# Kernel optimization log

Hardware: AMD Instinct MI355X
Metric: run time of the kernel (lower is better)

Reference implementation:

```python
import jax, jax.numpy as jnp
import numpy as np

B, K, N, D, H, NNEG, NTOP = 8, 8, 128, 256, 128, 64, 64
UNARY_SCALES = (1.0, 1.0, 1.0)  # one scale per tree level, tree_height = log2(K) = 3


def setup_inputs():
    key = jax.random.key(0)
    ks = jax.random.split(key, 8)
    s = 0.05
    return {
        'pos_fea': jax.random.normal(ks[0], (B, K, N, D), jnp.float32),
        'neg_fea': jax.random.normal(ks[1], (B * K, NNEG, D), jnp.float32),
        'pos_classes': jax.random.randint(ks[2], (B, K, N), 0, 20),
        'target_class': jax.random.randint(ks[3], (B,), 0, 20),
        'Wp1': jax.random.normal(ks[4], (2 * D, H), jnp.float32) * s,
        'bp1': jnp.zeros((H,), jnp.float32),
        'Wp2': jax.random.normal(ks[5], (H, 1), jnp.float32) * s,
        'bp2': jnp.zeros((1,), jnp.float32),
        'Wu1': jax.random.normal(ks[6], (2 * D, H), jnp.float32) * s,
        'bu1': jnp.zeros((H,), jnp.float32),
        'Wu2': jax.random.normal(ks[7], (H, 1), jnp.float32) * s,
        'bu2': jnp.zeros((1,), jnp.float32),
    }


def _relation(f0, f1, W1, b1, W2, b2):
    # RelationModule: Dense(H, relu) -> Dense(1) applied to concat([f0_m, f1_n])
    # for every cross pair; concat-Dense is split into two GEMMs. -> [Bn, M0, M1]
    d = f0.shape[-1]
    h0 = jnp.einsum('bmd,dh->bmh', f0, W1[:d])
    h1 = jnp.einsum('bnd,dh->bnh', f1, W1[d:])
    h = jax.nn.relu(h0[:, :, None, :] + h1[:, None, :, :] + b1)
    return jnp.einsum('bmnh,h->bmn', h, W2[:, 0]) + b2[0]


def _bg(t, idx):
    # batched_gather along axis 1: t [Bn, P, ...], idx [Bn, T]
    ie = idx.reshape(idx.shape + (1,) * (t.ndim - 2))
    ie = jnp.broadcast_to(ie, idx.shape + t.shape[2:])
    return jnp.take_along_axis(t, ie, axis=1)


def _rep(fea, sub):
    # subproblem representative feature: fea [Bn,S,N,D], sub [Bn,M,S] -> [Bn,M,D]
    idx = jnp.swapaxes(sub, 1, 2)[..., None]              # [Bn,S,M,1]
    idx = jnp.broadcast_to(idx, idx.shape[:-1] + (fea.shape[-1],))
    return jnp.take_along_axis(fea, idx, axis=2).mean(axis=1)


def _tree(pos_fea, neg_fea, Wp1, bp1, Wp2, bp2, Wu1, bu1, Wu2, bu2):
    pos_flat = pos_fea.reshape(B * K, N, D)
    # UnaryModule: mean relation score of each positive proposal vs the negative bag
    ue = _relation(pos_flat, neg_fea, Wu1, bu1, Wu2, bu2).mean(-1)   # [B*K, N]
    sub = jnp.broadcast_to(jnp.arange(N, dtype=jnp.int32)[None, :, None], (B * K, N, 1))
    pe = jnp.zeros_like(ue)
    tree_height = int(np.log2(K))
    best = None
    for i in range(tree_height):
        S = 2 ** i                      # subproblem size per branch at this level
        Bn = sub.shape[0] // 2
        M = sub.shape[1]
        sub2 = sub.reshape(Bn, 2, M, S)  # [::2] / [1::2] split of adjacent rows
        sub0, sub1 = sub2[:, 0], sub2[:, 1]
        pe2 = pe.reshape(Bn, 2, M)
        ue2 = ue.reshape(Bn, 2, M)
        fea = pos_flat.reshape(Bn, 2, S, N, D)
        rep0 = _rep(fea[:, 0], sub0)
        rep1 = _rep(fea[:, 1], sub1)
        # PairwiseCrossSimilarity: scores for all cross pairs of candidates
        scores = _relation(rep0, rep1, Wp1, bp1, Wp2, bp2).reshape(Bn, M * M)
        p0 = jnp.repeat(jnp.arange(M), M)
        p1 = jnp.tile(jnp.arange(M), M)
        pe = pe2[:, 0][:, p0] + pe2[:, 1][:, p1] - scores
        ue = ue2[:, 0][:, p0] + ue2[:, 1][:, p1]
        total = pe + UNARY_SCALES[i] * ue
        sub = jnp.concatenate([sub0[:, p0], sub1[:, p1]], axis=-1)  # [Bn, M*M, 2S]
        topk = 1 if i == tree_height - 1 else min(M * M, NTOP)
        _, inds = jax.lax.top_k(-total, topk)
        sub = _bg(sub, inds)
        ue = jnp.take_along_axis(ue, inds, axis=1)
        pe = jnp.take_along_axis(pe, inds, axis=1)
        best = jnp.take_along_axis(total, inds, axis=1)
    return sub, best


def reference(pos_fea, neg_fea, pos_classes, target_class,
              Wp1, bp1, Wp2, bp2, Wu1, bu1, Wu2, bu2):
    sub, _ = _tree(pos_fea, neg_fea, Wp1, bp1, Wp2, bp2, Wu1, bu1, Wu2, bu2)
    is_target = (pos_classes == target_class[:, None, None]).astype(jnp.float32)
    return sub[:, 0], is_target  # selected proposal per image [B,K], [B,K,N]
```

## Files before the change

kernel.cpp:

```cpp
#include <hip/hip_runtime.h>
#include <stdint.h>

#define B_ 8
#define K_ 8
#define N_ 128
#define D_ 256
#define H_ 128
#define NNEG_ 64

typedef unsigned long long u64;

__device__ __forceinline__ u64 shfl_xor_u64(u64 v, int m) {
    int lo = __shfl_xor((int)(unsigned)v, m, 64);
    int hi = __shfl_xor((int)(unsigned)(v >> 32), m, 64);
    return ((u64)(unsigned)hi << 32) | (unsigned)lo;
}
__device__ __forceinline__ u64 bitonic_merge64(u64 m, int lane) {
#pragma unroll
    for (int j = 32; j > 0; j >>= 1) {
        u64 o = shfl_xor_u64(m, j);
        bool keepMin = ((lane & j) == 0);
        bool lt = m < o;
        m = (keepMin == lt) ? m : o;
    }
    return m;
}
__device__ __forceinline__ unsigned sortable(float f) {
    unsigned u = __float_as_uint(f);
    return (u & 0x80000000u) ? ~u : (u | 0x80000000u);
}
__device__ __forceinline__ float unsortable(unsigned u) {
    return __uint_as_float((u & 0x80000000u) ? (u & 0x7FFFFFFFu) : ~u);
}
__device__ __forceinline__ void sort128_wave0(u64* cand, int cc, int lane) {
    u64 v0 = (lane < cc) ? cand[lane] : ~0ull;
    u64 v1 = (64 + lane < cc) ? cand[64 + lane] : ~0ull;
#pragma unroll
    for (int k = 2; k <= 64; k <<= 1) {
        bool d0 = ((lane & k) == 0);
        bool d1 = (k == 64) ? false : d0;
#pragma unroll
        for (int j = k >> 1; j > 0; j >>= 1) {
            u64 o0 = shfl_xor_u64(v0, j);
            bool km0 = (((lane & j) == 0) == d0);
            v0 = (km0 == (v0 < o0)) ? v0 : o0;
            u64 o1 = shfl_xor_u64(v1, j);
            bool km1 = (((lane & j) == 0) == d1);
            v1 = (km1 == (v1 < o1)) ? v1 : o1;
        }
    }
    if (v0 > v1) { u64 tmp = v0; v0 = v1; v1 = tmp; }
#pragma unroll
    for (int j = 32; j > 0; j >>= 1) {
        bool km = ((lane & j) == 0);
        u64 o0 = shfl_xor_u64(v0, j);
        v0 = (km == (v0 < o0)) ? v0 : o0;
        u64 o1 = shfl_xor_u64(v1, j);
        v1 = (km == (v1 < o1)) ? v1 : o1;
    }
    cand[lane] = v0; cand[64 + lane] = v1;
}

__global__ __launch_bounds__(256) void g1_gemm(
    const float* __restrict__ pos, const float* __restrict__ neg,
    const float* __restrict__ Wu1, const float* __restrict__ Wp1,
    const int* __restrict__ pos_classes, const int* __restrict__ target_class,
    float* __restrict__ HU0, float* __restrict__ HU1n,
    float* __restrict__ HP0, float* __restrict__ HP1,
    float* __restrict__ outp) {
    int bid = blockIdx.x;
    int t = threadIdx.x;
    if (bid >= 448) {
        int base = (bid - 448) * 2048 + t * 8;
#pragma unroll
        for (int q = 0; q < 8; ++q) {
            int idx = base + q;
            outp[64 + idx] = (pos_classes[idx] == target_class[idx >> 10]) ? 1.0f : 0.0f;
        }
        return;
    }
    const float* A; const float* W; float* OUT; int rb;
    if (bid < 128)      { A = pos; W = Wu1;           OUT = HU0;  rb = bid * 64; }
    else if (bid < 192) { A = neg; W = Wu1 + D_ * H_; OUT = HU1n; rb = (bid - 128) * 64; }
    else if (bid < 320) { A = pos; W = Wp1;           OUT = HP0;  rb = (bid - 192) * 64; }
    else                { A = pos; W = Wp1 + D_ * H_; OUT = HP1;  rb = (bid - 320) * 64; }

    __shared__ float As[64][17];
    __shared__ float Bs[16][128];
    int tx = t & 15, ty = t >> 4;
    float acc[4][8];
#pragma unroll
    for (int i = 0; i < 4; ++i)
#pragma unroll
        for (int j = 0; j < 8; ++j) acc[i][j] = 0.f;

    for (int k0 = 0; k0 < D_; k0 += 16) {
        {
            int row = t >> 2, kq = (t & 3) * 4;
            const float4 av = *(const float4*)&A[(size_t)(rb + row) * D_ + k0 + kq];
            As[row][kq + 0] = av.x; As[row][kq + 1] = av.y;
            As[row][kq + 2] = av.z; As[row][kq + 3] = av.w;
        }
        {
            int flat = t * 8;
            int kr = flat >> 7, hc = flat & 127;
            float4 b0 = *(const float4*)&W[(size_t)(k0 + kr) * H_ + hc];
            float4 b1 = *(const float4*)&W[(size_t)(k0 + kr) * H_ + hc + 4];
            *(float4*)&Bs[kr][hc] = b0;
            *(float4*)&Bs[kr][hc + 4] = b1;
        }
        __syncthreads();
#pragma unroll
        for (int kk = 0; kk < 16; ++kk) {
            float a0 = As[ty * 4 + 0][kk], a1 = As[ty * 4 + 1][kk];
            float a2 = As[ty * 4 + 2][kk], a3 = As[ty * 4 + 3][kk];
            float bv[8];
            *(float4*)&bv[0] = *(const float4*)&Bs[kk][tx * 8];
            *(float4*)&bv[4] = *(const float4*)&Bs[kk][tx * 8 + 4];
#pragma unroll
            for (int j = 0; j < 8; ++j) {
                acc[0][j] += a0 * bv[j];
                acc[1][j] += a1 * bv[j];
                acc[2][j] += a2 * bv[j];
                acc[3][j] += a3 * bv[j];
            }
        }
        __syncthreads();
    }
#pragma unroll
    for (int i = 0; i < 4; ++i) {
        float4 o0 = {acc[i][0], acc[i][1], acc[i][2], acc[i][3]};
        float4 o1 = {acc[i][4], acc[i][5], acc[i][6], acc[i][7]};
        *(float4*)&OUT[(size_t)(rb + ty * 4 + i) * H_ + tx * 8] = o0;
        *(float4*)&OUT[(size_t)(rb + ty * 4 + i) * H_ + tx * 8 + 4] = o1;
    }
}

__global__ __launch_bounds__(256) void g2_ue_sc0(
    const float* __restrict__ HU0, const float* __restrict__ HU1n,
    const float* __restrict__ bu1, const float* __restrict__ Wu2,
    const float* __restrict__ bu2v,
    const float* __restrict__ HP0, const float* __restrict__ HP1,
    const float* __restrict__ bp1, const float* __restrict__ Wp2,
    const float* __restrict__ bp2,
    float* __restrict__ t0, float* __restrict__ sc0) {
    __shared__ float smem[13568];
    float (*Ls)[129] = (float(*)[129])smem;
    float (*Rs)[129] = (float(*)[129])(smem + 4128);
    float* wsv = smem + 4128 + 8256;
    float (*red)[33] = (float(*)[33])(smem + 4128 + 8256 + 128);

    int bid = blockIdx.x;
    int t = threadIdx.x;
    bool is_ue = bid < 256;

    if (is_ue) {
        int bk = bid >> 2, mt = bid & 3;
        for (int i = t; i < 64 * 128; i += 256) {
            int n = i >> 7, h = i & 127;
            Rs[n][h] = HU1n[(size_t)(bk * NNEG_ + n) * H_ + h];
        }
        for (int i = t; i < 32 * 128; i += 256) {
            int m = i >> 7, h = i & 127;
            Ls[m][h] = HU0[(size_t)(bk * N_ + mt * 32 + m) * H_ + h] + bu1[h];
        }
        if (t < 128) wsv[t] = Wu2[t];
    } else {
        int bid2 = bid - 256;
        int b = bid2 >> 3, m0t = (bid2 >> 1) & 3, m1t = bid2 & 1;
        const float* Lg = HP0 + (size_t)b * 2 * N_ * H_ + m0t * 32 * H_;
        const float* Rg = HP1 + (size_t)b * 2 * N_ * H_ + N_ * H_ + m1t * 64 * H_;
        for (int i = t; i < 64 * 128; i += 256) {
            int n = i >> 7, h = i & 127;
            Rs[n][h] = Rg[(size_t)n * H_ + h];
        }
        for (int i = t; i < 32 * 128; i += 256) {
            int m = i >> 7, h = i & 127;
            Ls[m][h] = Lg[(size_t)m * H_ + h] + bp1[h];
        }
        if (t < 128) wsv[t] = Wp2[t];
    }
    __syncthreads();

    int tm = t & 7, tn = t >> 3;
    const float* l0 = &Ls[tm * 4 + 0][0];
    const float* l1 = &Ls[tm * 4 + 1][0];
    const float* l2 = &Ls[tm * 4 + 2][0];
    const float* l3 = &Ls[tm * 4 + 3][0];
    const float* r0 = &Rs[tn * 2 + 0][0];
    const float* r1 = &Rs[tn * 2 + 1][0];
    float a00 = 0.f, a01 = 0.f, a10 = 0.f, a11 = 0.f;
    float a20 = 0.f, a21 = 0.f, a30 = 0.f, a31 = 0.f;
#pragma unroll 4
    for (int h = 0; h < 128; ++h) {
        float w = wsv[h];
        float b0 = r0[h], b1 = r1[h];
        float a0 = l0[h], a1 = l1[h], a2 = l2[h], a3 = l3[h];
        float v;
        v = a0 + b0; v = v > 0.f ? v : 0.f; a00 += v * w;
        v = a0 + b1; v = v > 0.f ? v : 0.f; a01 += v * w;
        v = a1 + b0; v = v > 0.f ? v : 0.f; a10 += v * w;
        v = a1 + b1; v = v > 0.f ? v : 0.f; a11 += v * w;
        v = a2 + b0; v = v > 0.f ? v : 0.f; a20 += v * w;
        v = a2 + b1; v = v > 0.f ? v : 0.f; a21 += v * w;
        v = a3 + b0; v = v > 0.f ? v : 0.f; a30 += v * w;
        v = a3 + b1; v = v > 0.f ? v : 0.f; a31 += v * w;
    }

    if (is_ue) {
        int bk = bid >> 2, mt = bid & 3;
        red[tm * 4 + 0][tn] = a00 + a01;
        red[tm * 4 + 1][tn] = a10 + a11;
        red[tm * 4 + 2][tn] = a20 + a21;
        red[tm * 4 + 3][tn] = a30 + a31;
        __syncthreads();
        if (t < 32) {
            float s = 0.f;
            for (int q = 0; q < 32; ++q) s += red[t][q];
            t0[bk * N_ + mt * 32 + t] = s * (1.0f / NNEG_) + bu2v[0];
        }
    } else {
        int bid2 = bid - 256;
        int b = bid2 >> 3, m0t = (bid2 >> 1) & 3, m1t = bid2 & 1;
        float bp2v = bp2[0];
        float* orow = sc0 + (size_t)b * 16384;
        float accs[4][2] = {{a00, a01}, {a10, a11}, {a20, a21}, {a30, a31}};
#pragma unroll
        for (int i = 0; i < 4; ++i) {
            int m0 = m0t * 32 + tm * 4 + i;
#pragma unroll
            for (int j = 0; j < 2; ++j) {
                int m1 = m1t * 64 + tn * 2 + j;
                orow[m0 * 128 + m1] = accs[i][j] + bp2v;
            }
        }
    }
}

__global__ __launch_bounds__(1024) void g3_top0(const float* __restrict__ sc0,
                                                const float* __restrict__ t0,
                                                float* __restrict__ tA,
                                                int* __restrict__ pA) {
    int r = blockIdx.x;
    int t = threadIdx.x, lane = t & 63;
    __shared__ float tt[256];
    __shared__ unsigned cnt[16][2];
    __shared__ unsigned ccnt;
    __shared__ u64 cand[128];
    if (t < 256) tt[t] = t0[r * 256 + t];
    if (t < 32) cnt[t >> 1][t & 1] = 0u;
    if (t == 0) ccnt = 0u;
    __syncthreads();
    const float* row = sc0 + (size_t)r * 16384;
    unsigned sv[16];
#pragma unroll
    for (int j = 0; j < 16; ++j) {
        int idx = j * 1024 + t;
        float v = (tt[idx >> 7] + tt[128 + (idx & 127)]) - row[idx];
        sv[j] = sortable(v);
    }
    unsigned T = 0u;
#pragma unroll
    for (int it = 0; it < 16; ++it) {
        int p = 30 - 2 * it;
        unsigned C1 = T | (1u << p), C2 = T | (2u << p), C3 = T | (3u << p);
        unsigned c13 = 0u, c2 = 0u;
#pragma unroll
        for (int j = 0; j < 16; ++j) {
            c13 += (sv[j] < C1) ? 1u : 0u;
            c13 += (sv[j] < C3) ? 0x10000u : 0u;
            c2 += (sv[j] < C2) ? 1u : 0u;
        }
#pragma unroll
        for (int off = 32; off > 0; off >>= 1) {
            c13 += (unsigned)__shfl_xor((int)c13, off, 64);
            c2 += (unsigned)__shfl_xor((int)c2, off, 64);
        }
        if (lane == 0) { atomicAdd(&cnt[it][0], c13); atomicAdd(&cnt[it][1], c2); }
        __syncthreads();
        unsigned t13 = cnt[it][0], t2v = cnt[it][1];
        unsigned t1 = t13 & 0xFFFFu, t3 = t13 >> 16;
        unsigned k = (t3 < 64u) ? 3u : (t2v < 64u) ? 2u : (t1 < 64u) ? 1u : 0u;
        T |= (k << p);
    }
#pragma unroll
    for (int j = 0; j < 16; ++j) {
        if (sv[j] <= T) {
            unsigned pos = atomicAdd(&ccnt, 1u);
            if (pos < 128u) {
                int idx = j * 1024 + t;
                cand[pos] = ((u64)sv[j] << 32) | (unsigned)idx;
            }
        }
    }
    __syncthreads();
    if (t < 64) {
        int cc = (int)(ccnt < 128u ? ccnt : 128u);
        sort128_wave0(cand, cc, lane);
        u64 kk = cand[lane];
        int idx = (int)(kk & 0xFFFFFFFFull);
        tA[r * 64 + lane] = unsortable((unsigned)(kk >> 32));
        pA[r * 64 + lane] = ((idx >> 7) << 8) | (idx & 127);
    }
}

__global__ __launch_bounds__(256) void g4a_s1(
    const float* __restrict__ HP0, const float* __restrict__ HP1,
    const float* __restrict__ tA, const int* __restrict__ pA,
    const float* __restrict__ bp1, const float* __restrict__ Wp2,
    const float* __restrict__ bp2, u64* __restrict__ g4top) {
    int bid = blockIdx.x;
    int u = bid >> 1, half = bid & 1;
    int t = threadIdx.x, lane = t & 63, w = t >> 6;
    __shared__ float LsT[128][68];
    __shared__ float RsT[128][36];
    __shared__ float taL[64], taR[64];
    __shared__ int paL[64], paR[64];
    __shared__ float wsv[128];
    __shared__ unsigned cnt[16][2];
    __shared__ unsigned ccnt;
    __shared__ u64 cand[128];
    if (t < 64) { taL[t] = tA[(2 * u) * 64 + t]; paL[t] = pA[(2 * u) * 64 + t]; }
    else if (t < 128) { int e = t - 64; taR[e] = tA[(2 * u + 1) * 64 + e]; paR[e] = pA[(2 * u + 1) * 64 + e]; }
    if (t < 128) wsv[t] = Wp2[t];
    if (t < 32) cnt[t >> 1][t & 1] = 0u;
    if (t == 0) ccnt = 0u;
    float bp2v = bp2[0];
    __syncthreads();
    for (int i = t; i < 64 * 128; i += 256) {
        int m = i >> 7, h = i & 127;
        int pk = paL[m]; int a0 = pk >> 8, a1 = pk & 255;
        float s = HP0[(size_t)(4 * u) * 16384 + a0 * 128 + h]
                + HP0[(size_t)(4 * u + 1) * 16384 + a1 * 128 + h];
        LsT[h][m] = s * 0.5f + bp1[h];
    }
    for (int i = t; i < 32 * 128; i += 256) {
        int n = i >> 7, h = i & 127;
        int ng = half * 32 + n;
        int pk = paR[ng]; int c0 = pk >> 8, c1 = pk & 255;
        float s = HP1[(size_t)(4 * u + 2) * 16384 + c0 * 128 + h]
                + HP1[(size_t)(4 * u + 3) * 16384 + c1 * 128 + h];
        RsT[h][n] = s * 0.5f;
    }
    __syncthreads();
    int qm = w * 4 + (lane >> 4);
    int qn = lane & 15;
    float acc[4][2];
#pragma unroll
    for (int i = 0; i < 4; ++i) { acc[i][0] = 0.f; acc[i][1] = 0.f; }
#pragma unroll 2
    for (int h = 0; h < 128; ++h) {
        float4 lv = *(const float4*)&LsT[h][qm * 4];
        float2 rv = *(const float2*)&RsT[h][qn * 2];
        float wv = wsv[h];
        float v;
        v = lv.x + rv.x; v = v > 0.f ? v : 0.f; acc[0][0] += v * wv;
        v = lv.x + rv.y; v = v > 0.f ? v : 0.f; acc[0][1] += v * wv;
        v = lv.y + rv.x; v = v > 0.f ? v : 0.f; acc[1][0] += v * wv;
        v = lv.y + rv.y; v = v > 0.f ? v : 0.f; acc[1][1] += v * wv;
        v = lv.z + rv.x; v = v > 0.f ? v : 0.f; acc[2][0] += v * wv;
        v = lv.z + rv.y; v = v > 0.f ? v : 0.f; acc[2][1] += v * wv;
        v = lv.w + rv.x; v = v > 0.f ? v : 0.f; acc[3][0] += v * wv;
        v = lv.w + rv.y; v = v > 0.f ? v : 0.f; acc[3][1] += v * wv;
    }
    unsigned sv[8];
#pragma unroll
    for (int mi = 0; mi < 4; ++mi) {
#pragma unroll
        for (int nj = 0; nj < 2; ++nj) {
            int m = qm * 4 + mi;
            int ng = half * 32 + qn * 2 + nj;
            float val = (taL[m] + taR[ng]) - (acc[mi][nj] + bp2v);
            sv[mi * 2 + nj] = sortable(val);
        }
    }
    unsigned T = 0u;
#pragma unroll
    for (int it = 0; it < 16; ++it) {
        int p = 30 - 2 * it;
        unsigned C1 = T | (1u << p), C2 = T | (2u << p), C3 = T | (3u << p);
        unsigned c13 = 0u, c2 = 0u;
#pragma unroll
        for (int j = 0; j < 8; ++j) {
            c13 += (sv[j] < C1) ? 1u : 0u;
            c13 += (sv[j] < C3) ? 0x10000u : 0u;
            c2 += (sv[j] < C2) ? 1u : 0u;
        }
#pragma unroll
        for (int off = 32; off > 0; off >>= 1) {
            c13 += (unsigned)__shfl_xor((int)c13, off, 64);
            c2 += (unsigned)__shfl_xor((int)c2, off, 64);
        }
        if (lane == 0) { atomicAdd(&cnt[it][0], c13); atomicAdd(&cnt[it][1], c2); }
        __syncthreads();
        unsigned t13 = cnt[it][0], t2v = cnt[it][1];
        unsigned t1 = t13 & 0xFFFFu, t3 = t13 >> 16;
        unsigned k = (t3 < 64u) ? 3u : (t2v < 64u) ? 2u : (t1 < 64u) ? 1u : 0u;
        T |= (k << p);
    }
#pragma unroll
    for (int j = 0; j < 8; ++j) {
        if (sv[j] <= T) {
            unsigned pos = atomicAdd(&ccnt, 1u);
            if (pos < 128u) {
                int mi = j >> 1, nj = j & 1;
                int idx = (qm * 4 + mi) * 64 + half * 32 + qn * 2 + nj;
                cand[pos] = ((u64)sv[j] << 32) | (unsigned)idx;
            }
        }
    }
    __syncthreads();
    if (w == 0) {
        int cc = (int)(ccnt < 128u ? ccnt : 128u);
        sort128_wave0(cand, cc, lane);
        g4top[(size_t)bid * 64 + lane] = cand[lane];
    }
}

__global__ __launch_bounds__(256) void g4b_s2(
    const float* __restrict__ HP0, const float* __restrict__ HP1,
    const int* __restrict__ pA, const u64* __restrict__ g4top,
    const float* __restrict__ bp1, const float* __restrict__ Wp2,
    const float* __restrict__ bp2, float* __restrict__ outp) {
    int b = blockIdx.x;
    int t = threadIdx.x, lane = t & 63, w = t >> 6;
    __shared__ float LsT[128][68];
    __shared__ float RsT[128][36];
    __shared__ float tL[64], tR[64];
    __shared__ unsigned subL[64], subR[64];
    __shared__ float wsv[128];
    __shared__ u64 sred[4];
    if (t < 128) wsv[t] = Wp2[t];
    float bp2v = bp2[0];
    if (w < 2) {
        const u64* A = g4top + (size_t)(4 * b + 2 * w) * 64;
        const u64* Bp = g4top + (size_t)(4 * b + 2 * w + 1) * 64;
        u64 x = A[lane], y = Bp[63 - lane];
        u64 m = x < y ? x : y;
        m = bitonic_merge64(m, lane);
        int idx = (int)(m & 0xFFFFFFFFull);
        int p0 = idx >> 6, p1 = idx & 63;
        float val = unsortable((unsigned)(m >> 32));
        int rowL = 4 * b + 2 * w;
        int pkL = pA[rowL * 64 + p0];
        int pkR = pA[(rowL + 1) * 64 + p1];
        unsigned leaves = ((unsigned)pkL << 16) | (unsigned)pkR;
        if (w == 0) { tL[lane] = val; subL[lane] = leaves; }
        else        { tR[lane] = val; subR[lane] = leaves; }
    }
    __syncthreads();
    for (int i = t; i < 64 * 128; i += 256) {
        int m = i >> 7, h = i & 127;
        unsigned s4 = subL[m];
        float s = HP0[(size_t)(8 * b + 0) * 16384 + ((s4 >> 24) & 255u) * 128 + h]
                + HP0[(size_t)(8 * b + 1) * 16384 + ((s4 >> 16) & 255u) * 128 + h]
                + HP0[(size_t)(8 * b + 2) * 16384 + ((s4 >> 8) & 255u) * 128 + h]
                + HP0[(size_t)(8 * b + 3) * 16384 + (s4 & 255u) * 128 + h];
        LsT[h][m] = s * 0.25f + bp1[h];
    }
    u64 best = ~0ull;
    int qm = w * 4 + (lane >> 4);
    int qn = lane & 15;
    for (int half = 0; half < 2; ++half) {
        __syncthreads();
        for (int i = t; i < 32 * 128; i += 256) {
            int n = i >> 7, h = i & 127;
            int ng = half * 32 + n;
            unsigned s4 = subR[ng];
            float s = HP1[(size_t)(8 * b + 4) * 16384 + ((s4 >> 24) & 255u) * 128 + h]
                    + HP1[(size_t)(8 * b + 5) * 16384 + ((s4 >> 16) & 255u) * 128 + h]
                    + HP1[(size_t)(8 * b + 6) * 16384 + ((s4 >> 8) & 255u) * 128 + h]
                    + HP1[(size_t)(8 * b + 7) * 16384 + (s4 & 255u) * 128 + h];
            RsT[h][n] = s * 0.25f;
        }
        __syncthreads();
        float acc[4][2];
#pragma unroll
        for (int i = 0; i < 4; ++i) { acc[i][0] = 0.f; acc[i][1] = 0.f; }
#pragma unroll 2
        for (int h = 0; h < 128; ++h) {
            float4 lv = *(const float4*)&LsT[h][qm * 4];
            float2 rv = *(const float2*)&RsT[h][qn * 2];
            float wv = wsv[h];
            float v;
            v = lv.x + rv.x; v = v > 0.f ? v : 0.f; acc[0][0] += v * wv;
            v = lv.x + rv.y; v = v > 0.f ? v : 0.f; acc[0][1] += v * wv;
            v = lv.y + rv.x; v = v > 0.f ? v : 0.f; acc[1][0] += v * wv;
            v = lv.y + rv.y; v = v > 0.f ? v : 0.f; acc[1][1] += v * wv;
            v = lv.z + rv.x; v = v > 0.f ? v : 0.f; acc[2][0] += v * wv;
            v = lv.z + rv.y; v = v > 0.f ? v : 0.f; acc[2][1] += v * wv;
            v = lv.w + rv.x; v = v > 0.f ? v : 0.f; acc[3][0] += v * wv;
            v = lv.w + rv.y; v = v > 0.f ? v : 0.f; acc[3][1] += v * wv;
        }
#pragma unroll
        for (int mi = 0; mi < 4; ++mi) {
#pragma unroll
            for (int nj = 0; nj < 2; ++nj) {
                int m = qm * 4 + mi;
                int ng = half * 32 + qn * 2 + nj;
                float val = (tL[m] + tR[ng]) - (acc[mi][nj] + bp2v);
                u64 kk = ((u64)sortable(val) << 32) | (unsigned)(m * 64 + ng);
                best = kk < best ? kk : best;
            }
        }
    }
#pragma unroll
    for (int off = 32; off > 0; off >>= 1) {
        u64 o = shfl_xor_u64(best, off);
        best = o < best ? o : best;
    }
    if (lane == 0) sred[w] = best;
    __syncthreads();
    if (t == 0) {
        u64 bb = sred[0];
        for (int p = 1; p < 4; ++p) { u64 o = sred[p]; bb = o < bb ? o : bb; }
        int idx = (int)(bb & 0xFFFFFFFFull);
        unsigned sl = subL[idx >> 6], sr = subR[idx & 63];
        outp[b * 8 + 0] = (float)((sl >> 24) & 255u);
        outp[b * 8 + 1] = (float)((sl >> 16) & 255u);
        outp[b * 8 + 2] = (float)((sl >> 8) & 255u);
        outp[b * 8 + 3] = (float)(sl & 255u);
        outp[b * 8 + 4] = (float)((sr >> 24) & 255u);
        outp[b * 8 + 5] = (float)((sr >> 16) & 255u);
        outp[b * 8 + 6] = (float)((sr >> 8) & 255u);
        outp[b * 8 + 7] = (float)(sr & 255u);
    }
}

extern "C" void kernel_launch(void* const* d_in, const int* in_sizes, int n_in,
                              void* d_out, int out_size, void* d_ws, size_t ws_size,
                              hipStream_t stream) {
    const float* pos = (const float*)d_in[0];
    const float* neg = (const float*)d_in[1];
    const int* pos_classes = (const int*)d_in[2];
    const int* target_class = (const int*)d_in[3];
    const float* Wp1 = (const float*)d_in[4];
    const float* bp1 = (const float*)d_in[5];
    const float* Wp2 = (const float*)d_in[6];
    const float* bp2 = (const float*)d_in[7];
    const float* Wu1 = (const float*)d_in[8];
    const float* bu1 = (const float*)d_in[9];
    const float* Wu2 = (const float*)d_in[10];
    const float* bu2 = (const float*)d_in[11];

    float* wsf = (float*)d_ws;
    float* HU0 = wsf;
    float* HP0 = HU0 + 1048576;
    float* HP1 = HP0 + 1048576;
    float* HU1n = HP1 + 1048576;
    float* t0 = HU1n + 524288;
    float* sc0 = t0 + 8192;
    float* tA = sc0 + 524288;
    int* pA = (int*)(tA + 2048);
    u64* g4top = (u64*)(pA + 2048);
    float* outp = (float*)d_out;

    g1_gemm<<<452, 256, 0, stream>>>(pos, neg, Wu1, Wp1, pos_classes,
                                     target_class, HU0, HU1n, HP0, HP1, outp);
    g2_ue_sc0<<<512, 256, 0, stream>>>(HU0, HU1n, bu1, Wu2, bu2,
                                       HP0, HP1, bp1, Wp2, bp2, t0, sc0);
    g3_top0<<<32, 1024, 0, stream>>>(sc0, t0, tA, pA);
    g4a_s1<<<32, 256, 0, stream>>>(HP0, HP1, tA, pA, bp1, Wp2, bp2, g4top);
    g4b_s2<<<8, 256, 0, stream>>>(HP0, HP1, pA, g4top, bp1, Wp2, bp2, outp);
}
```

Before: 207.9 us.

## Enlarge GEMM tiles to 128 rows and vectorize LDS reads in GEMM and pair-score kernels

The first GEMM kernel now computes 128-row tiles with an 8x8 register tile per thread, halving its grid. It loads A and W with float4 stores into padded shared memory and reads A fragments as float4 across k. The pair-score kernel switches to float4 shared-memory reads over h, with row-strided thread mapping and padded 132-wide rows. The aim is fewer LDS instructions per FMA and more operand reuse, at the cost of higher register pressure and fewer blocks (228) to fill the CUs.

```diff
diff --git a/kernel.cpp b/kernel.cpp
--- a/kernel.cpp
+++ b/kernel.cpp
@@ -70,8 +70,8 @@
     float* __restrict__ outp) {
     int bid = blockIdx.x;
     int t = threadIdx.x;
-    if (bid >= 448) {
-        int base = (bid - 448) * 2048 + t * 8;
+    if (bid >= 224) {
+        int base = (bid - 224) * 2048 + t * 8;
 #pragma unroll
         for (int q = 0; q < 8; ++q) {
             int idx = base + q;
@@ -80,59 +80,69 @@
         return;
     }
     const float* A; const float* W; float* OUT; int rb;
-    if (bid < 128)      { A = pos; W = Wu1;           OUT = HU0;  rb = bid * 64; }
-    else if (bid < 192) { A = neg; W = Wu1 + D_ * H_; OUT = HU1n; rb = (bid - 128) * 64; }
-    else if (bid < 320) { A = pos; W = Wp1;           OUT = HP0;  rb = (bid - 192) * 64; }
-    else                { A = pos; W = Wp1 + D_ * H_; OUT = HP1;  rb = (bid - 320) * 64; }
-
-    __shared__ float As[64][17];
-    __shared__ float Bs[16][128];
+    if (bid < 64)       { A = pos; W = Wu1;           OUT = HU0;  rb = bid * 128; }
+    else if (bid < 96)  { A = neg; W = Wu1 + D_ * H_; OUT = HU1n; rb = (bid - 64) * 128; }
+    else if (bid < 160) { A = pos; W = Wp1;           OUT = HP0;  rb = (bid - 96) * 128; }
+    else                { A = pos; W = Wp1 + D_ * H_; OUT = HP1;  rb = (bid - 160) * 128; }
+
+    __shared__ float As[128][20];
+    __shared__ float Bs[16][132];
     int tx = t & 15, ty = t >> 4;
-    float acc[4][8];
-#pragma unroll
-    for (int i = 0; i < 4; ++i)
+    float acc[8][8];
+#pragma unroll
+    for (int i = 0; i < 8; ++i)
 #pragma unroll
         for (int j = 0; j < 8; ++j) acc[i][j] = 0.f;
 
     for (int k0 = 0; k0 < D_; k0 += 16) {
-        {
-            int row = t >> 2, kq = (t & 3) * 4;
-            const float4 av = *(const float4*)&A[(size_t)(rb + row) * D_ + k0 + kq];
-            As[row][kq + 0] = av.x; As[row][kq + 1] = av.y;
-            As[row][kq + 2] = av.z; As[row][kq + 3] = av.w;
-        }
-        {
-            int flat = t * 8;
-            int kr = flat >> 7, hc = flat & 127;
-            float4 b0 = *(const float4*)&W[(size_t)(k0 + kr) * H_ + hc];
-            float4 b1 = *(const float4*)&W[(size_t)(k0 + kr) * H_ + hc + 4];
-            *(float4*)&Bs[kr][hc] = b0;
-            *(float4*)&Bs[kr][hc + 4] = b1;
-        }
-        __syncthreads();
-#pragma unroll
-        for (int kk = 0; kk < 16; ++kk) {
-            float a0 = As[ty * 4 + 0][kk], a1 = As[ty * 4 + 1][kk];
-            float a2 = As[ty * 4 + 2][kk], a3 = As[ty * 4 + 3][kk];
-            float bv[8];
-            *(float4*)&bv[0] = *(const float4*)&Bs[kk][tx * 8];
-            *(float4*)&bv[4] = *(const float4*)&Bs[kk][tx * 8 + 4];
-#pragma unroll
-            for (int j = 0; j < 8; ++j) {
-                acc[0][j] += a0 * bv[j];
-                acc[1][j] += a1 * bv[j];
-                acc[2][j] += a2 * bv[j];
-                acc[3][j] += a3 * bv[j];
+#pragma unroll
+        for (int q = 0; q < 2; ++q) {
+            int f = q * 256 + t;
+            int row = f >> 2, kq = (f & 3) * 4;
+            *(float4*)&As[row][kq] =
+                *(const float4*)&A[(size_t)(rb + row) * D_ + k0 + kq];
+            int kr = f >> 5, hc = (f & 31) * 4;
+            *(float4*)&Bs[kr][hc] =
+                *(const float4*)&W[(size_t)(k0 + kr) * H_ + hc];
+        }
+        __syncthreads();
+#pragma unroll
+        for (int kq = 0; kq < 16; kq += 4) {
+            float4 af[8];
+#pragma unroll
+            for (int i = 0; i < 8; ++i)
+                af[i] = *(const float4*)&As[ty + 16 * i][kq];
+            float4 b0[4], b1[4];
+#pragma unroll
+            for (int j = 0; j < 4; ++j) {
+                b0[j] = *(const float4*)&Bs[kq + j][tx * 8];
+                b1[j] = *(const float4*)&Bs[kq + j][tx * 8 + 4];
             }
-        }
-        __syncthreads();
-    }
-#pragma unroll
-    for (int i = 0; i < 4; ++i) {
+#pragma unroll
+            for (int j = 0; j < 4; ++j) {
+#pragma unroll
+                for (int i = 0; i < 8; ++i) {
+                    float a = (&af[i].x)[j];
+                    acc[i][0] += a * b0[j].x;
+                    acc[i][1] += a * b0[j].y;
+                    acc[i][2] += a * b0[j].z;
+                    acc[i][3] += a * b0[j].w;
+                    acc[i][4] += a * b1[j].x;
+                    acc[i][5] += a * b1[j].y;
+                    acc[i][6] += a * b1[j].z;
+                    acc[i][7] += a * b1[j].w;
+                }
+            }
+        }
+        __syncthreads();
+    }
+#pragma unroll
+    for (int i = 0; i < 8; ++i) {
+        int row = rb + ty + 16 * i;
         float4 o0 = {acc[i][0], acc[i][1], acc[i][2], acc[i][3]};
         float4 o1 = {acc[i][4], acc[i][5], acc[i][6], acc[i][7]};
-        *(float4*)&OUT[(size_t)(rb + ty * 4 + i) * H_ + tx * 8] = o0;
-        *(float4*)&OUT[(size_t)(rb + ty * 4 + i) * H_ + tx * 8 + 4] = o1;
+        *(float4*)&OUT[(size_t)row * H_ + tx * 8] = o0;
+        *(float4*)&OUT[(size_t)row * H_ + tx * 8 + 4] = o1;
     }
 }
 
@@ -144,11 +154,10 @@
     const float* __restrict__ bp1, const float* __restrict__ Wp2,
     const float* __restrict__ bp2,
     float* __restrict__ t0, float* __restrict__ sc0) {
-    __shared__ float smem[13568];
-    float (*Ls)[129] = (float(*)[129])smem;
-    float (*Rs)[129] = (float(*)[129])(smem + 4128);
-    float* wsv = smem + 4128 + 8256;
-    float (*red)[33] = (float(*)[33])(smem + 4128 + 8256 + 128);
+    __shared__ float Ls[32][132];
+    __shared__ float Rs[64][132];
+    __shared__ float wsv[128];
+    __shared__ float red[32][33];
 
     int bid = blockIdx.x;
     int t = threadIdx.x;
@@ -183,36 +192,41 @@
     __syncthreads();
 
     int tm = t & 7, tn = t >> 3;
-    const float* l0 = &Ls[tm * 4 + 0][0];
-    const float* l1 = &Ls[tm * 4 + 1][0];
-    const float* l2 = &Ls[tm * 4 + 2][0];
-    const float* l3 = &Ls[tm * 4 + 3][0];
-    const float* r0 = &Rs[tn * 2 + 0][0];
-    const float* r1 = &Rs[tn * 2 + 1][0];
     float a00 = 0.f, a01 = 0.f, a10 = 0.f, a11 = 0.f;
     float a20 = 0.f, a21 = 0.f, a30 = 0.f, a31 = 0.f;
-#pragma unroll 4
-    for (int h = 0; h < 128; ++h) {
-        float w = wsv[h];
-        float b0 = r0[h], b1 = r1[h];
-        float a0 = l0[h], a1 = l1[h], a2 = l2[h], a3 = l3[h];
-        float v;
-        v = a0 + b0; v = v > 0.f ? v : 0.f; a00 += v * w;
-        v = a0 + b1; v = v > 0.f ? v : 0.f; a01 += v * w;
-        v = a1 + b0; v = v > 0.f ? v : 0.f; a10 += v * w;
-        v = a1 + b1; v = v > 0.f ? v : 0.f; a11 += v * w;
-        v = a2 + b0; v = v > 0.f ? v : 0.f; a20 += v * w;
-        v = a2 + b1; v = v > 0.f ? v : 0.f; a21 += v * w;
-        v = a3 + b0; v = v > 0.f ? v : 0.f; a30 += v * w;
-        v = a3 + b1; v = v > 0.f ? v : 0.f; a31 += v * w;
+#pragma unroll 2
+    for (int h = 0; h < 128; h += 4) {
+        float4 wv = *(const float4*)&wsv[h];
+        float4 r0 = *(const float4*)&Rs[tn * 2][h];
+        float4 r1 = *(const float4*)&Rs[tn * 2 + 1][h];
+        float4 l0 = *(const float4*)&Ls[tm][h];
+        float4 l1 = *(const float4*)&Ls[tm + 8][h];
+        float4 l2 = *(const float4*)&Ls[tm + 16][h];
+        float4 l3 = *(const float4*)&Ls[tm + 24][h];
+#pragma unroll
+        for (int c = 0; c < 4; ++c) {
+            float w = (&wv.x)[c];
+            float b0 = (&r0.x)[c], b1 = (&r1.x)[c];
+            float x0 = (&l0.x)[c], x1 = (&l1.x)[c];
+            float x2 = (&l2.x)[c], x3 = (&l3.x)[c];
+            float v;
+            v = x0 + b0; v = v > 0.f ? v : 0.f; a00 += v * w;
+            v = x0 + b1; v = v > 0.f ? v : 0.f; a01 += v * w;
+            v = x1 + b0; v = v > 0.f ? v : 0.f; a10 += v * w;
+            v = x1 + b1; v = v > 0.f ? v : 0.f; a11 += v * w;
+            v = x2 + b0; v = v > 0.f ? v : 0.f; a20 += v * w;
+            v = x2 + b1; v = v > 0.f ? v : 0.f; a21 += v * w;
+            v = x3 + b0; v = v > 0.f ? v : 0.f; a30 += v * w;
+            v = x3 + b1; v = v > 0.f ? v : 0.f; a31 += v * w;
+        }
     }
 
     if (is_ue) {
         int bk = bid >> 2, mt = bid & 3;
-        red[tm * 4 + 0][tn] = a00 + a01;
-        red[tm * 4 + 1][tn] = a10 + a11;
-        red[tm * 4 + 2][tn] = a20 + a21;
-        red[tm * 4 + 3][tn] = a30 + a31;
+        red[tm + 0][tn] = a00 + a01;
+        red[tm + 8][tn] = a10 + a11;
+        red[tm + 16][tn] = a20 + a21;
+        red[tm + 24][tn] = a30 + a31;
         __syncthreads();
         if (t < 32) {
             float s = 0.f;
@@ -227,7 +241,7 @@
         float accs[4][2] = {{a00, a01}, {a10, a11}, {a20, a21}, {a30, a31}};
 #pragma unroll
         for (int i = 0; i < 4; ++i) {
-            int m0 = m0t * 32 + tm * 4 + i;
+            int m0 = m0t * 32 + tm + 8 * i;
 #pragma unroll
             for (int j = 0; j < 2; ++j) {
                 int m1 = m1t * 64 + tn * 2 + j;
@@ -555,7 +569,7 @@
     u64* g4top = (u64*)(pA + 2048);
     float* outp = (float*)d_out;
 
-    g1_gemm<<<452, 256, 0, stream>>>(pos, neg, Wu1, Wp1, pos_classes,
+    g1_gemm<<<228, 256, 0, stream>>>(pos, neg, Wu1, Wp1, pos_classes,
                                      target_class, HU0, HU1n, HP0, HP1, outp);
     g2_ue_sc0<<<512, 256, 0, stream>>>(HU0, HU1n, bu1, Wu2, bu2,
                                        HP0, HP1, bp1, Wp2, bp2, t0, sc0);
```

New measurement: 224.0 us. +7.7%, slower.
